# Performance work log

Hardware: AMD Instinct MI355X
Metric: run time of the kernel (lower is better)

## Reference

```python
import jax, jax.numpy as jnp
import numpy as np

N = 50000          # nodes
E = 1600000        # edges (avg degree 32)
B = 64             # graphs in batch
IN_CH = 128
HEADS = 8
HD = 8             # head_dim = ceil(64/8)
GH = HEADS * HD    # 64 = gat_hidden_dim
HIDDEN = 64
NC = 10
NEG_SLOPE = 0.2
BN_EPS = 1e-5
SIGMA = 0.5


def setup_inputs() -> dict:
    key = jax.random.key(0)
    ks = jax.random.split(key, 24)
    s = 0.1
    inp = {
        "x": jax.random.normal(ks[0], (N, IN_CH), jnp.float32),
        "raw_x": jax.random.uniform(ks[1], (N, 3), jnp.float32),
        "edge_index": jax.random.randint(ks[2], (2, E), 0, N, jnp.int32),
        "batch": jnp.sort(jax.random.randint(ks[3], (N,), 0, B, jnp.int32)),
        # conv1 (heads=8, out=8, edge_dim=1)
        "W1": jax.random.normal(ks[4], (IN_CH, GH), jnp.float32) * s,
        "att_src1": jax.random.normal(ks[5], (HEADS, HD), jnp.float32) * s,
        "att_dst1": jax.random.normal(ks[6], (HEADS, HD), jnp.float32) * s,
        "We1": jax.random.normal(ks[7], (1, GH), jnp.float32) * s,
        "att_e1": jax.random.normal(ks[8], (HEADS, HD), jnp.float32) * s,
        "b1": jax.random.normal(ks[9], (GH,), jnp.float32) * s,
        "gamma1": jnp.ones((GH,), jnp.float32),
        "beta1": jnp.zeros((GH,), jnp.float32),
        "rm1": jax.random.normal(ks[10], (GH,), jnp.float32) * s,
        "rv1": jax.random.uniform(ks[11], (GH,), jnp.float32) + 0.5,
        # conv2 (heads=1, out=64, edge_dim=1)
        "W2": jax.random.normal(ks[12], (GH, HIDDEN), jnp.float32) * s,
        "att_src2": jax.random.normal(ks[13], (1, HIDDEN), jnp.float32) * s,
        "att_dst2": jax.random.normal(ks[14], (1, HIDDEN), jnp.float32) * s,
        "We2": jax.random.normal(ks[15], (1, HIDDEN), jnp.float32) * s,
        "att_e2": jax.random.normal(ks[16], (1, HIDDEN), jnp.float32) * s,
        "b2": jax.random.normal(ks[17], (HIDDEN,), jnp.float32) * s,
        "gamma2": jnp.ones((HIDDEN,), jnp.float32),
        "beta2": jnp.zeros((HIDDEN,), jnp.float32),
        "rm2": jax.random.normal(ks[18], (HIDDEN,), jnp.float32) * s,
        "rv2": jax.random.uniform(ks[19], (HIDDEN,), jnp.float32) + 0.5,
        # classifier
        "Wc": jax.random.normal(ks[20], (HIDDEN, NC), jnp.float32) * s,
        "bc": jax.random.normal(ks[21], (NC,), jnp.float32) * s,
    }
    return inp


def _gat_conv(x, src, dst, edge_attr, W, a_src, a_dst, W_e, a_e, bias, heads, out_ch, n):
    """PyG GATConv (concat=True, add_self_loops=True, fill_value='mean', eval mode)."""
    e0 = edge_attr.shape[0]
    # self-loop edge_attr = mean of incoming edge_attr per node (0 if isolated)
    cnt = jax.ops.segment_sum(jnp.ones((e0,), x.dtype), dst, num_segments=n)
    loop_attr = jax.ops.segment_sum(edge_attr, dst, num_segments=n) / jnp.maximum(cnt, 1.0)[:, None]
    loops = jnp.arange(n, dtype=src.dtype)
    src2 = jnp.concatenate([src, loops])
    dst2 = jnp.concatenate([dst, loops])
    ea = jnp.concatenate([edge_attr, loop_attr], axis=0)          # [E2, 1]
    h = (x @ W).reshape(n, heads, out_ch)                          # [N, H, D]
    al_s = (h * a_src).sum(-1)                                     # [N, H]
    al_d = (h * a_dst).sum(-1)                                     # [N, H]
    al_e = ((ea @ W_e).reshape(-1, heads, out_ch) * a_e).sum(-1)   # [E2, H]
    logits = al_s[src2] + al_d[dst2] + al_e                        # [E2, H]
    logits = jnp.where(logits >= 0, logits, NEG_SLOPE * logits)    # leaky_relu
    # segment softmax over destination nodes (every node has a self loop)
    m = jax.ops.segment_max(logits, dst2, num_segments=n)
    ex = jnp.exp(logits - m[dst2])
    alpha = ex / jax.ops.segment_sum(ex, dst2, num_segments=n)[dst2]
    out = jax.ops.segment_sum(h[src2] * alpha[:, :, None], dst2, num_segments=n)
    return out.reshape(n, heads * out_ch) + bias


def _bn_eval(x, gamma, beta, rm, rv):
    return (x - rm) * (gamma / jnp.sqrt(rv + BN_EPS)) + beta


def reference(x, raw_x, edge_index, batch,
              W1, att_src1, att_dst1, We1, att_e1, b1, gamma1, beta1, rm1, rv1,
              W2, att_src2, att_dst2, We2, att_e2, b2, gamma2, beta2, rm2, rv2,
              Wc, bc):
    src, dst = edge_index[0], edge_index[1]
    # gaussian edge weights from raw features
    diff = raw_x[src] - raw_x[dst]
    dist2 = (diff * diff).sum(axis=1)
    edge_w = jnp.exp(-dist2 / (2.0 * SIGMA * SIGMA))[:, None]      # [E, 1]
    # eval mode: dropout is identity
    h = _gat_conv(x, src, dst, edge_w, W1, att_src1, att_dst1, We1, att_e1, b1, HEADS, HD, N)
    h = jax.nn.elu(_bn_eval(h, gamma1, beta1, rm1, rv1))
    h = _gat_conv(h, src, dst, edge_w, W2, att_src2, att_dst2, We2, att_e2, b2, 1, HIDDEN, N)
    h = jax.nn.elu(_bn_eval(h, gamma2, beta2, rm2, rv2))
    # global mean pool over graphs
    cnt = jax.ops.segment_sum(jnp.ones((N,), h.dtype), batch, num_segments=B)
    g = jax.ops.segment_sum(h, batch, num_segments=B) / jnp.maximum(cnt, 1.0)[:, None]
    return g @ Wc + bc
```

## Files before the change

kernel.cpp:

```cpp
#include <hip/hip_runtime.h>
#include <math.h>

#define N_NODES 50000
#define N_EDGES 1600000
#define NBATCH  64
#define INCH    128
#define HEADS   8
#define HD      8
#define GH      64
#define HIDDEN  64
#define NC      10
#define NEG_SLOPE 0.2f
#define BN_EPS  1e-5f

#define SCAN_TPB 1024
#define NTILES   ((N_NODES + SCAN_TPB - 1) / SCAN_TPB)

typedef unsigned short ushort_t;
typedef unsigned int uint_t;

__device__ __forceinline__ ushort_t f2bf(float f) {
  uint_t u = __float_as_uint(f);
  uint_t r = (u + 0x7fffu + ((u >> 16) & 1u)) >> 16;
  return (ushort_t)r;
}
__device__ __forceinline__ float2 upk(uint_t u) {
  return make_float2(__uint_as_float(u << 16), __uint_as_float(u & 0xffff0000u));
}

__global__ __launch_bounds__(256) void edge_kernel(
    const int* __restrict__ ei, const float* __restrict__ raw,
    float* __restrict__ ea, float* __restrict__ easum, int* __restrict__ cnt) {
  int e = blockIdx.x * blockDim.x + threadIdx.x;
  if (e >= N_EDGES) return;
  int s = ei[e], d = ei[N_EDGES + e];
  float dx = raw[s*3+0] - raw[d*3+0];
  float dy = raw[s*3+1] - raw[d*3+1];
  float dz = raw[s*3+2] - raw[d*3+2];
  float w = __expf(-2.0f * (dx*dx + dy*dy + dz*dz));
  ea[e] = w;
  atomicAdd(&easum[d], w);
  atomicAdd(&cnt[d], 1);
}

__global__ __launch_bounds__(SCAN_TPB) void scan_part(
    const int* __restrict__ cnt, const float* __restrict__ easum,
    int* __restrict__ rowptr, float* __restrict__ loopat, int* __restrict__ bsum) {
  __shared__ int s[SCAN_TPB];
  int t = threadIdx.x;
  int i = blockIdx.x * SCAN_TPB + t;
  int v = (i < N_NODES) ? cnt[i] : 0;
  s[t] = v; __syncthreads();
  for (int off = 1; off < SCAN_TPB; off <<= 1) {
    int u = (t >= off) ? s[t - off] : 0;
    __syncthreads();
    s[t] += u;
    __syncthreads();
  }
  if (i < N_NODES) {
    rowptr[i] = s[t] - v;
    loopat[i] = easum[i] / fmaxf((float)v, 1.0f);
  }
  if (t == SCAN_TPB - 1) bsum[blockIdx.x] = s[t];
}

__global__ __launch_bounds__(64) void scan_top(int* __restrict__ bsum, int* __restrict__ rowptr) {
  int t = threadIdx.x;
  int v = (t < NTILES) ? bsum[t] : 0;
  int orig = v;
  for (int off = 1; off < 64; off <<= 1) {
    int u = __shfl_up(v, off);
    if (t >= off) v += u;
  }
  if (t < NTILES) bsum[t] = v - orig;
  if (t == 0) rowptr[N_NODES] = N_EDGES;
}

__global__ __launch_bounds__(SCAN_TPB) void scan_add(int* __restrict__ rowptr, const int* __restrict__ bsum) {
  int i = blockIdx.x * SCAN_TPB + threadIdx.x;
  if (i < N_NODES) rowptr[i] += bsum[blockIdx.x];
}

__global__ __launch_bounds__(256) void scatter_kernel(
    const int* __restrict__ ei, const float* __restrict__ ea,
    const int* __restrict__ rowptr, int* __restrict__ cnt2,
    int* __restrict__ csr_src, float* __restrict__ csr_ea) {
  int e = blockIdx.x * blockDim.x + threadIdx.x;
  if (e >= N_EDGES) return;
  int s = ei[e], d = ei[N_EDGES + e];
  int pos = rowptr[d] + atomicAdd(&cnt2[d], 1);
  csr_src[pos] = s;
  csr_ea[pos] = ea[e];
}

__global__ __launch_bounds__(256) void gemm1_kernel(
    const float* __restrict__ x, const float* __restrict__ W1,
    ushort_t* __restrict__ h1b) {
  __shared__ float w[INCH * GH];
  for (int i = threadIdx.x; i < INCH * GH / 4; i += blockDim.x)
    ((float4*)w)[i] = ((const float4*)W1)[i];
  __syncthreads();
  int lane = threadIdx.x & 63;
  int waveG = __builtin_amdgcn_readfirstlane((blockIdx.x * blockDim.x + threadIdx.x) >> 6);
  int nWaves = (gridDim.x * blockDim.x) >> 6;
  for (int base = waveG * 4; base < N_NODES; base += nWaves * 4) {
    float acc[4] = {0.f, 0.f, 0.f, 0.f};
    #pragma unroll 8
    for (int k = 0; k < INCH; ++k) {
      float wv = w[k * GH + lane];
      #pragma unroll
      for (int j = 0; j < 4; ++j)
        acc[j] = fmaf(x[(size_t)(base + j) * INCH + k], wv, acc[j]);
    }
    #pragma unroll
    for (int j = 0; j < 4; ++j)
      h1b[(size_t)(base + j) * GH + lane] = f2bf(acc[j]);
  }
}

__global__ __launch_bounds__(256) void conv1_kernel(
    const ushort_t* __restrict__ h1b,
    const float* __restrict__ asrc, const float* __restrict__ adst,
    const float* __restrict__ We, const float* __restrict__ ae,
    const int* __restrict__ rowptr,
    const int* __restrict__ csr_src, const float* __restrict__ csr_ea,
    const float* __restrict__ loopat, const float* __restrict__ bias,
    const float* __restrict__ gamma, const float* __restrict__ beta,
    const float* __restrict__ rm, const float* __restrict__ rv,
    float* __restrict__ h2) {
  __shared__ int   src_lds[4][64];
  __shared__ float ea_lds[4][64];
  int l = threadIdx.x & 63;
  int w = threadIdx.x >> 6;
  int n = blockIdx.x * 4 + w;
  if (n >= N_NODES) return;
  int i = l & 15;
  int q = l >> 4;
  const float4 as4 = ((const float4*)asrc)[i];
  const float4 ad4 = ((const float4*)adst)[i];
  float4 we4 = ((const float4*)We)[i];
  float4 ae4 = ((const float4*)ae)[i];
  float ce = we4.x*ae4.x + we4.y*ae4.y + we4.z*ae4.z + we4.w*ae4.w;
  ce += __shfl_xor(ce, 1);
  const uint2* tab = (const uint2*)h1b;
  uint2 uself = tab[(size_t)n * 16 + i];
  float2 s01 = upk(uself.x), s23 = upk(uself.y);
  float als_s = s01.x*as4.x + s01.y*as4.y + s23.x*as4.z + s23.y*as4.w;
  als_s += __shfl_xor(als_s, 1);
  float aldn  = s01.x*ad4.x + s01.y*ad4.y + s23.x*ad4.z + s23.y*ad4.w;
  aldn += __shfl_xor(aldn, 1);
  int jb = rowptr[n], je = rowptr[n + 1];
  float m = -1e30f, ssum = 0.f;
  float a0 = 0.f, a1 = 0.f, a2 = 0.f, a3 = 0.f;
  for (int cb = jb; cb < je; cb += 64) {
    int cnt = je - cb; if (cnt > 64) cnt = 64;
    int idx = cb + l;
    bool vld = l < cnt;
    src_lds[w][l] = vld ? csr_src[idx] : 0;
    ea_lds[w][l]  = vld ? csr_ea[idx] : 0.f;
    int nb = (cnt + 3) >> 2;
    int j0 = q;
    int s0 = (j0 < cnt) ? src_lds[w][j0] : 0;
    uint2 rcur = tab[(size_t)s0 * 16 + i];
    for (int b = 0; b < nb; ++b) {
      uint2 rnext = rcur;
      if (b + 1 < nb) {
        int jn = ((b + 1) << 2) + q;
        int sn = (jn < cnt) ? src_lds[w][jn] : 0;
        rnext = tab[(size_t)sn * 16 + i];
      }
      int j = (b << 2) + q;
      bool val = j < cnt;
      float eav = val ? ea_lds[w][j] : 0.f;
      float2 p01 = upk(rcur.x), p23 = upk(rcur.y);
      float dp = p01.x*as4.x + p01.y*as4.y + p23.x*as4.z + p23.y*as4.w;
      dp += __shfl_xor(dp, 1);
      float lg = dp + aldn + eav * ce;
      lg = (lg >= 0.f) ? lg : NEG_SLOPE * lg;
      lg = val ? lg : -1e30f;
      float bm = fmaxf(lg, __shfl_xor(lg, 16));
      bm = fmaxf(bm, __shfl_xor(bm, 32));
      float nm = fmaxf(m, bm);
      float sc = __expf(m - nm);
      float p  = __expf(lg - nm);
      float ps = p;
      ps += __shfl_xor(ps, 16);
      ps += __shfl_xor(ps, 32);
      ssum = ssum * sc + ps;
      m = nm;
      a0 = a0 * sc + p * p01.x;
      a1 = a1 * sc + p * p01.y;
      a2 = a2 * sc + p * p23.x;
      a3 = a3 * sc + p * p23.y;
      rcur = rnext;
    }
  }
  a0 += __shfl_xor(a0, 16); a0 += __shfl_xor(a0, 32);
  a1 += __shfl_xor(a1, 16); a1 += __shfl_xor(a1, 32);
  a2 += __shfl_xor(a2, 16); a2 += __shfl_xor(a2, 32);
  a3 += __shfl_xor(a3, 16); a3 += __shfl_xor(a3, 32);
  {
    float lg = als_s + aldn + loopat[n] * ce;
    lg = (lg >= 0.f) ? lg : NEG_SLOPE * lg;
    float nm = fmaxf(m, lg);
    float sc = __expf(m - nm);
    float p  = __expf(lg - nm);
    ssum = ssum * sc + p;
    a0 = a0 * sc + p * s01.x;
    a1 = a1 * sc + p * s01.y;
    a2 = a2 * sc + p * s23.x;
    a3 = a3 * sc + p * s23.y;
  }
  float inv = 1.0f / ssum;
  float4 b4 = ((const float4*)bias)[i];
  float4 g4 = ((const float4*)gamma)[i];
  float4 be4 = ((const float4*)beta)[i];
  float4 rm4 = ((const float4*)rm)[i];
  float4 rv4 = ((const float4*)rv)[i];
  float o0 = a0 * inv + b4.x, o1 = a1 * inv + b4.y;
  float o2 = a2 * inv + b4.z, o3 = a3 * inv + b4.w;
  o0 = (o0 - rm4.x) * (g4.x * rsqrtf(rv4.x + BN_EPS)) + be4.x;
  o1 = (o1 - rm4.y) * (g4.y * rsqrtf(rv4.y + BN_EPS)) + be4.y;
  o2 = (o2 - rm4.z) * (g4.z * rsqrtf(rv4.z + BN_EPS)) + be4.z;
  o3 = (o3 - rm4.w) * (g4.w * rsqrtf(rv4.w + BN_EPS)) + be4.w;
  o0 = (o0 > 0.f) ? o0 : expm1f(o0);
  o1 = (o1 > 0.f) ? o1 : expm1f(o1);
  o2 = (o2 > 0.f) ? o2 : expm1f(o2);
  o3 = (o3 > 0.f) ? o3 : expm1f(o3);
  if (q == 0)
    ((float4*)(h2 + (size_t)n * GH))[i] = make_float4(o0, o1, o2, o3);
}

__global__ __launch_bounds__(256) void gemm2_kernel(
    const float* __restrict__ x, const float* __restrict__ W2,
    ushort_t* __restrict__ h2mb) {
  __shared__ float w[HIDDEN * HIDDEN];
  for (int i = threadIdx.x; i < HIDDEN * HIDDEN / 4; i += blockDim.x)
    ((float4*)w)[i] = ((const float4*)W2)[i];
  __syncthreads();
  int lane = threadIdx.x & 63;
  int waveG = __builtin_amdgcn_readfirstlane((blockIdx.x * blockDim.x + threadIdx.x) >> 6);
  int nWaves = (gridDim.x * blockDim.x) >> 6;
  for (int base = waveG * 4; base < N_NODES; base += nWaves * 4) {
    float acc[4] = {0.f, 0.f, 0.f, 0.f};
    #pragma unroll 8
    for (int k = 0; k < HIDDEN; ++k) {
      float wv = w[k * HIDDEN + lane];
      #pragma unroll
      for (int j = 0; j < 4; ++j)
        acc[j] = fmaf(x[(size_t)(base + j) * HIDDEN + k], wv, acc[j]);
    }
    #pragma unroll
    for (int j = 0; j < 4; ++j)
      h2mb[(size_t)(base + j) * HIDDEN + lane] = f2bf(acc[j]);
  }
}

__global__ __launch_bounds__(256) void conv2_kernel(
    const ushort_t* __restrict__ h2mb,
    const float* __restrict__ asrc, const float* __restrict__ adst,
    const float* __restrict__ We, const float* __restrict__ ae,
    const int* __restrict__ rowptr,
    const int* __restrict__ csr_src, const float* __restrict__ csr_ea,
    const float* __restrict__ loopat, const float* __restrict__ bias,
    const float* __restrict__ gamma, const float* __restrict__ beta,
    const float* __restrict__ rm, const float* __restrict__ rv,
    const int* __restrict__ batch,
    float* __restrict__ pool, int* __restrict__ cntg) {
  __shared__ int   src_lds[4][64];
  __shared__ float ea_lds[4][64];
  int l = threadIdx.x & 63;
  int w = threadIdx.x >> 6;
  int n = blockIdx.x * 4 + w;
  if (n >= N_NODES) return;
  int i = l & 15;
  int q = l >> 4;
  const float4 as4 = ((const float4*)asrc)[i];
  const float4 ad4 = ((const float4*)adst)[i];
  float4 we4 = ((const float4*)We)[i];
  float4 ae4 = ((const float4*)ae)[i];
  float ce = we4.x*ae4.x + we4.y*ae4.y + we4.z*ae4.z + we4.w*ae4.w;
  ce += __shfl_xor(ce, 1); ce += __shfl_xor(ce, 2);
  ce += __shfl_xor(ce, 4); ce += __shfl_xor(ce, 8);
  const uint2* tab = (const uint2*)h2mb;
  uint2 uself = tab[(size_t)n * 16 + i];
  float2 s01 = upk(uself.x), s23 = upk(uself.y);
  float als_s = s01.x*as4.x + s01.y*as4.y + s23.x*as4.z + s23.y*as4.w;
  als_s += __shfl_xor(als_s, 1); als_s += __shfl_xor(als_s, 2);
  als_s += __shfl_xor(als_s, 4); als_s += __shfl_xor(als_s, 8);
  float aldn  = s01.x*ad4.x + s01.y*ad4.y + s23.x*ad4.z + s23.y*ad4.w;
  aldn += __shfl_xor(aldn, 1); aldn += __shfl_xor(aldn, 2);
  aldn += __shfl_xor(aldn, 4); aldn += __shfl_xor(aldn, 8);
  int jb = rowptr[n], je = rowptr[n + 1];
  float m = -1e30f, ssum = 0.f;
  float a0 = 0.f, a1 = 0.f, a2 = 0.f, a3 = 0.f;
  for (int cb = jb; cb < je; cb += 64) {
    int cnt = je - cb; if (cnt > 64) cnt = 64;
    int idx = cb + l;
    bool vld = l < cnt;
    src_lds[w][l] = vld ? csr_src[idx] : 0;
    ea_lds[w][l]  = vld ? csr_ea[idx] : 0.f;
    int nb = (cnt + 3) >> 2;
    int j0 = q;
    int s0 = (j0 < cnt) ? src_lds[w][j0] : 0;
    uint2 rcur = tab[(size_t)s0 * 16 + i];
    for (int b = 0; b < nb; ++b) {
      uint2 rnext = rcur;
      if (b + 1 < nb) {
        int jn = ((b + 1) << 2) + q;
        int sn = (jn < cnt) ? src_lds[w][jn] : 0;
        rnext = tab[(size_t)sn * 16 + i];
      }
      int j = (b << 2) + q;
      bool val = j < cnt;
      float eav = val ? ea_lds[w][j] : 0.f;
      float2 p01 = upk(rcur.x), p23 = upk(rcur.y);
      float dp = p01.x*as4.x + p01.y*as4.y + p23.x*as4.z + p23.y*as4.w;
      dp += __shfl_xor(dp, 1); dp += __shfl_xor(dp, 2);
      dp += __shfl_xor(dp, 4); dp += __shfl_xor(dp, 8);
      float lg = dp + aldn + eav * ce;
      lg = (lg >= 0.f) ? lg : NEG_SLOPE * lg;
      lg = val ? lg : -1e30f;
      float bm = fmaxf(lg, __shfl_xor(lg, 16));
      bm = fmaxf(bm, __shfl_xor(bm, 32));
      float nm = fmaxf(m, bm);
      float sc = __expf(m - nm);
      float p  = __expf(lg - nm);
      float ps = p;
      ps += __shfl_xor(ps, 16);
      ps += __shfl_xor(ps, 32);
      ssum = ssum * sc + ps;
      m = nm;
      a0 = a0 * sc + p * p01.x;
      a1 = a1 * sc + p * p01.y;
      a2 = a2 * sc + p * p23.x;
      a3 = a3 * sc + p * p23.y;
      rcur = rnext;
    }
  }
  a0 += __shfl_xor(a0, 16); a0 += __shfl_xor(a0, 32);
  a1 += __shfl_xor(a1, 16); a1 += __shfl_xor(a1, 32);
  a2 += __shfl_xor(a2, 16); a2 += __shfl_xor(a2, 32);
  a3 += __shfl_xor(a3, 16); a3 += __shfl_xor(a3, 32);
  {
    float lg = als_s + aldn + loopat[n] * ce;
    lg = (lg >= 0.f) ? lg : NEG_SLOPE * lg;
    float nm = fmaxf(m, lg);
    float sc = __expf(m - nm);
    float p  = __expf(lg - nm);
    ssum = ssum * sc + p;
    a0 = a0 * sc + p * s01.x;
    a1 = a1 * sc + p * s01.y;
    a2 = a2 * sc + p * s23.x;
    a3 = a3 * sc + p * s23.y;
  }
  float inv = 1.0f / ssum;
  float4 b4 = ((const float4*)bias)[i];
  float4 g4 = ((const float4*)gamma)[i];
  float4 be4 = ((const float4*)beta)[i];
  float4 rm4 = ((const float4*)rm)[i];
  float4 rv4 = ((const float4*)rv)[i];
  float o0 = a0 * inv + b4.x, o1 = a1 * inv + b4.y;
  float o2 = a2 * inv + b4.z, o3 = a3 * inv + b4.w;
  o0 = (o0 - rm4.x) * (g4.x * rsqrtf(rv4.x + BN_EPS)) + be4.x;
  o1 = (o1 - rm4.y) * (g4.y * rsqrtf(rv4.y + BN_EPS)) + be4.y;
  o2 = (o2 - rm4.z) * (g4.z * rsqrtf(rv4.z + BN_EPS)) + be4.z;
  o3 = (o3 - rm4.w) * (g4.w * rsqrtf(rv4.w + BN_EPS)) + be4.w;
  o0 = (o0 > 0.f) ? o0 : expm1f(o0);
  o1 = (o1 > 0.f) ? o1 : expm1f(o1);
  o2 = (o2 > 0.f) ? o2 : expm1f(o2);
  o3 = (o3 > 0.f) ? o3 : expm1f(o3);
  if (q == 0) {
    int b = batch[n];
    float* pp = pool + (size_t)b * HIDDEN + 4 * i;
    atomicAdd(pp + 0, o0);
    atomicAdd(pp + 1, o1);
    atomicAdd(pp + 2, o2);
    atomicAdd(pp + 3, o3);
    if (l == 0) atomicAdd(&cntg[b], 1);
  }
}

__global__ __launch_bounds__(640) void final_kernel(
    const float* __restrict__ pool, const int* __restrict__ cntg,
    const float* __restrict__ Wc, const float* __restrict__ bc,
    float* __restrict__ out) {
  int t = threadIdx.x;
  if (t >= NBATCH * NC) return;
  int b = t / NC, c = t - b * NC;
  float inv = 1.0f / fmaxf((float)cntg[b], 1.0f);
  float s = bc[c];
  #pragma unroll
  for (int d = 0; d < HIDDEN; ++d)
    s = fmaf(pool[b * HIDDEN + d] * inv, Wc[d * NC + c], s);
  out[t] = s;
}

extern "C" void kernel_launch(void* const* d_in, const int* in_sizes, int n_in,
                              void* d_out, int out_size, void* d_ws, size_t ws_size,
                              hipStream_t stream) {
  const float* x     = (const float*)d_in[0];
  const float* raw   = (const float*)d_in[1];
  const int*   ei    = (const int*)  d_in[2];
  const int*   batch = (const int*)  d_in[3];
  const float* W1    = (const float*)d_in[4];
  const float* asrc1 = (const float*)d_in[5];
  const float* adst1 = (const float*)d_in[6];
  const float* We1   = (const float*)d_in[7];
  const float* ae1   = (const float*)d_in[8];
  const float* b1    = (const float*)d_in[9];
  const float* g1    = (const float*)d_in[10];
  const float* be1   = (const float*)d_in[11];
  const float* rm1   = (const float*)d_in[12];
  const float* rv1   = (const float*)d_in[13];
  const float* W2    = (const float*)d_in[14];
  const float* asrc2 = (const float*)d_in[15];
  const float* adst2 = (const float*)d_in[16];
  const float* We2   = (const float*)d_in[17];
  const float* ae2   = (const float*)d_in[18];
  const float* b2    = (const float*)d_in[19];
  const float* g2    = (const float*)d_in[20];
  const float* be2   = (const float*)d_in[21];
  const float* rm2   = (const float*)d_in[22];
  const float* rv2   = (const float*)d_in[23];
  const float* Wc    = (const float*)d_in[24];
  const float* bc    = (const float*)d_in[25];
  float* out = (float*)d_out;

  char* ws = (char*)d_ws;
  size_t off = 0;
  auto alloc = [&](size_t bytes) -> void* {
    void* p = ws + off;
    off += bytes;
    off = (off + 255) & ~(size_t)255;
    return p;
  };
  float*    ea      = (float*)   alloc((size_t)N_EDGES * 4);
  float*    csr_ea  = (float*)   alloc((size_t)N_EDGES * 4);
  int*      csr_src = (int*)     alloc((size_t)N_EDGES * 4);
  float*    easum   = (float*)   alloc((size_t)N_NODES * 4);
  int*      cnt     = (int*)     alloc((size_t)N_NODES * 4);
  int*      cnt2    = (int*)     alloc((size_t)N_NODES * 4);
  int*      rowptr  = (int*)     alloc((size_t)(N_NODES + 1) * 4);
  float*    loopat  = (float*)   alloc((size_t)N_NODES * 4);
  ushort_t* h1b     = (ushort_t*)alloc((size_t)N_NODES * GH * 2);
  float*    h2      = (float*)   alloc((size_t)N_NODES * GH * 4);
  ushort_t* h2mb    = (ushort_t*)alloc((size_t)N_NODES * HIDDEN * 2);
  int*      bsum    = (int*)     alloc(64 * 4);
  float*    pool    = (float*)   alloc((size_t)NBATCH * HIDDEN * 4);
  int*      cntg    = (int*)     alloc((size_t)NBATCH * 4);

  hipMemsetAsync(easum, 0, (size_t)N_NODES * 4, stream);
  hipMemsetAsync(cnt,   0, (size_t)N_NODES * 4, stream);
  hipMemsetAsync(cnt2,  0, (size_t)N_NODES * 4, stream);
  hipMemsetAsync(pool,  0, (size_t)NBATCH * HIDDEN * 4, stream);
  hipMemsetAsync(cntg,  0, (size_t)NBATCH * 4, stream);

  int egrid = (N_EDGES + 255) / 256;
  edge_kernel<<<egrid, 256, 0, stream>>>(ei, raw, ea, easum, cnt);
  scan_part<<<NTILES, SCAN_TPB, 0, stream>>>(cnt, easum, rowptr, loopat, bsum);
  scan_top<<<1, 64, 0, stream>>>(bsum, rowptr);
  scan_add<<<NTILES, SCAN_TPB, 0, stream>>>(rowptr, bsum);
  scatter_kernel<<<egrid, 256, 0, stream>>>(ei, ea, rowptr, cnt2, csr_src, csr_ea);

  gemm1_kernel<<<1024, 256, 0, stream>>>(x, W1, h1b);
  conv1_kernel<<<(N_NODES + 3) / 4, 256, 0, stream>>>(h1b, asrc1, adst1, We1, ae1,
      rowptr, csr_src, csr_ea, loopat, b1, g1, be1, rm1, rv1, h2);
  gemm2_kernel<<<1024, 256, 0, stream>>>(h2, W2, h2mb);
  conv2_kernel<<<(N_NODES + 3) / 4, 256, 0, stream>>>(h2mb, asrc2, adst2, We2, ae2,
      rowptr, csr_src, csr_ea, loopat, b2, g2, be2, rm2, rv2, batch, pool, cntg);
  final_kernel<<<1, 640, 0, stream>>>(pool, cntg, Wc, bc, out);
}
```

Measured before the change: 929.9 us.

## Precompute per-node attention scores in GEMMs and drop online softmax max tracking

```diff
diff --git a/kernel.cpp b/kernel.cpp
--- a/kernel.cpp
+++ b/kernel.cpp
@@ -95,7 +95,8 @@
 
 __global__ __launch_bounds__(256) void gemm1_kernel(
     const float* __restrict__ x, const float* __restrict__ W1,
-    ushort_t* __restrict__ h1b) {
+    const float* __restrict__ asrc, const float* __restrict__ adst,
+    ushort_t* __restrict__ h1b, float* __restrict__ als, float* __restrict__ ald) {
   __shared__ float w[INCH * GH];
   for (int i = threadIdx.x; i < INCH * GH / 4; i += blockDim.x)
     ((float4*)w)[i] = ((const float4*)W1)[i];
@@ -103,6 +104,8 @@
   int lane = threadIdx.x & 63;
   int waveG = __builtin_amdgcn_readfirstlane((blockIdx.x * blockDim.x + threadIdx.x) >> 6);
   int nWaves = (gridDim.x * blockDim.x) >> 6;
+  float a_s = asrc[lane];
+  float a_d = adst[lane];
   for (int base = waveG * 4; base < N_NODES; base += nWaves * 4) {
     float acc[4] = {0.f, 0.f, 0.f, 0.f};
     #pragma unroll 8
@@ -113,14 +116,24 @@
         acc[j] = fmaf(x[(size_t)(base + j) * INCH + k], wv, acc[j]);
     }
     #pragma unroll
-    for (int j = 0; j < 4; ++j)
-      h1b[(size_t)(base + j) * GH + lane] = f2bf(acc[j]);
+    for (int j = 0; j < 4; ++j) {
+      int n = base + j;
+      float hv = acc[j];
+      h1b[(size_t)n * GH + lane] = f2bf(hv);
+      float ps = hv * a_s, pd = hv * a_d;
+      ps += __shfl_xor(ps, 1); ps += __shfl_xor(ps, 2); ps += __shfl_xor(ps, 4);
+      pd += __shfl_xor(pd, 1); pd += __shfl_xor(pd, 2); pd += __shfl_xor(pd, 4);
+      if ((lane & 7) == 0) {
+        als[n * HEADS + (lane >> 3)] = ps;
+        ald[n * HEADS + (lane >> 3)] = pd;
+      }
+    }
   }
 }
 
 __global__ __launch_bounds__(256) void conv1_kernel(
-    const ushort_t* __restrict__ h1b,
-    const float* __restrict__ asrc, const float* __restrict__ adst,
+    const ushort_t* __restrict__ h1b, const float* __restrict__ als,
+    const float* __restrict__ ald,
     const float* __restrict__ We, const float* __restrict__ ae,
     const int* __restrict__ rowptr,
     const int* __restrict__ csr_src, const float* __restrict__ csr_ea,
@@ -136,104 +149,111 @@
   if (n >= N_NODES) return;
   int i = l & 15;
   int q = l >> 4;
-  const float4 as4 = ((const float4*)asrc)[i];
-  const float4 ad4 = ((const float4*)adst)[i];
+  int head = i >> 1;
   float4 we4 = ((const float4*)We)[i];
   float4 ae4 = ((const float4*)ae)[i];
   float ce = we4.x*ae4.x + we4.y*ae4.y + we4.z*ae4.z + we4.w*ae4.w;
   ce += __shfl_xor(ce, 1);
+  float aldn = ald[(size_t)n * HEADS + head];
+  float als_self = als[(size_t)n * HEADS + head];
   const uint2* tab = (const uint2*)h1b;
   uint2 uself = tab[(size_t)n * 16 + i];
   float2 s01 = upk(uself.x), s23 = upk(uself.y);
-  float als_s = s01.x*as4.x + s01.y*as4.y + s23.x*as4.z + s23.y*as4.w;
-  als_s += __shfl_xor(als_s, 1);
-  float aldn  = s01.x*ad4.x + s01.y*ad4.y + s23.x*ad4.z + s23.y*ad4.w;
-  aldn += __shfl_xor(aldn, 1);
   int jb = rowptr[n], je = rowptr[n + 1];
-  float m = -1e30f, ssum = 0.f;
+  float ssum = 0.f;
   float a0 = 0.f, a1 = 0.f, a2 = 0.f, a3 = 0.f;
+
+#define C1_LOADS(J, R, A, E)                                           \
+  {                                                                    \
+    int jj = (J);                                                      \
+    bool vv = jj < cnt;                                                \
+    int ss = vv ? src_lds[w][jj] : 0;                                  \
+    R = tab[(size_t)ss * 16 + i];                                      \
+    A = vv ? als[(size_t)ss * HEADS + head] : -1e30f;                  \
+    E = vv ? ea_lds[w][jj] : 0.f;                                      \
+  }
+#define C1_LOADG(GI, R0,R1,R2,R3, A0,A1,A2,A3, E0,E1,E2,E3)            \
+  {                                                                    \
+    int jbase = (GI) * 16 + q;                                         \
+    C1_LOADS(jbase,      R0, A0, E0)                                   \
+    C1_LOADS(jbase + 4,  R1, A1, E1)                                   \
+    C1_LOADS(jbase + 8,  R2, A2, E2)                                   \
+    C1_LOADS(jbase + 12, R3, A3, E3)                                   \
+  }
+#define C1_PROC(R, A, E)                                               \
+  {                                                                    \
+    float2 t01 = upk(R.x), t23 = upk(R.y);                             \
+    float lg = A + aldn + E * ce;                                      \
+    lg = (lg >= 0.f) ? lg : NEG_SLOPE * lg;                            \
+    float p = __expf(fminf(lg, 60.f));                                 \
+    ssum += p;                                                         \
+    a0 = fmaf(p, t01.x, a0); a1 = fmaf(p, t01.y, a1);                  \
+    a2 = fmaf(p, t23.x, a2); a3 = fmaf(p, t23.y, a3);                  \
+  }
+
   for (int cb = jb; cb < je; cb += 64) {
     int cnt = je - cb; if (cnt > 64) cnt = 64;
-    int idx = cb + l;
-    bool vld = l < cnt;
-    src_lds[w][l] = vld ? csr_src[idx] : 0;
-    ea_lds[w][l]  = vld ? csr_ea[idx] : 0.f;
-    int nb = (cnt + 3) >> 2;
-    int j0 = q;
-    int s0 = (j0 < cnt) ? src_lds[w][j0] : 0;
-    uint2 rcur = tab[(size_t)s0 * 16 + i];
-    for (int b = 0; b < nb; ++b) {
-      uint2 rnext = rcur;
-      if (b + 1 < nb) {
-        int jn = ((b + 1) << 2) + q;
-        int sn = (jn < cnt) ? src_lds[w][jn] : 0;
-        rnext = tab[(size_t)sn * 16 + i];
+    src_lds[w][l] = (l < cnt) ? csr_src[cb + l] : 0;
+    ea_lds[w][l]  = (l < cnt) ? csr_ea[cb + l] : 0.f;
+    int ng = (cnt + 15) >> 4;
+    uint2 rA0, rA1, rA2, rA3, rB0, rB1, rB2, rB3;
+    float aA0, aA1, aA2, aA3, aB0, aB1, aB2, aB3;
+    float eA0, eA1, eA2, eA3, eB0, eB1, eB2, eB3;
+    C1_LOADG(0, rA0,rA1,rA2,rA3, aA0,aA1,aA2,aA3, eA0,eA1,eA2,eA3)
+    for (int gi = 0; gi < ng; gi += 2) {
+      bool hasB = (gi + 1) < ng;
+      if (hasB) C1_LOADG(gi + 1, rB0,rB1,rB2,rB3, aB0,aB1,aB2,aB3, eB0,eB1,eB2,eB3)
+      C1_PROC(rA0, aA0, eA0) C1_PROC(rA1, aA1, eA1)
+      C1_PROC(rA2, aA2, eA2) C1_PROC(rA3, aA3, eA3)
+      if (hasB) {
+        if (gi + 2 < ng) C1_LOADG(gi + 2, rA0,rA1,rA2,rA3, aA0,aA1,aA2,aA3, eA0,eA1,eA2,eA3)
+        C1_PROC(rB0, aB0, eB0) C1_PROC(rB1, aB1, eB1)
+        C1_PROC(rB2, aB2, eB2) C1_PROC(rB3, aB3, eB3)
       }
-      int j = (b << 2) + q;
-      bool val = j < cnt;
-      float eav = val ? ea_lds[w][j] : 0.f;
-      float2 p01 = upk(rcur.x), p23 = upk(rcur.y);
-      float dp = p01.x*as4.x + p01.y*as4.y + p23.x*as4.z + p23.y*as4.w;
-      dp += __shfl_xor(dp, 1);
-      float lg = dp + aldn + eav * ce;
-      lg = (lg >= 0.f) ? lg : NEG_SLOPE * lg;
-      lg = val ? lg : -1e30f;
-      float bm = fmaxf(lg, __shfl_xor(lg, 16));
-      bm = fmaxf(bm, __shfl_xor(bm, 32));
-      float nm = fmaxf(m, bm);
-      float sc = __expf(m - nm);
-      float p  = __expf(lg - nm);
-      float ps = p;
-      ps += __shfl_xor(ps, 16);
-      ps += __shfl_xor(ps, 32);
-      ssum = ssum * sc + ps;
-      m = nm;
-      a0 = a0 * sc + p * p01.x;
-      a1 = a1 * sc + p * p01.y;
-      a2 = a2 * sc + p * p23.x;
-      a3 = a3 * sc + p * p23.y;
-      rcur = rnext;
     }
   }
+#undef C1_LOADS
+#undef C1_LOADG
+#undef C1_PROC
+
+  ssum += __shfl_xor(ssum, 16); ssum += __shfl_xor(ssum, 32);
   a0 += __shfl_xor(a0, 16); a0 += __shfl_xor(a0, 32);
   a1 += __shfl_xor(a1, 16); a1 += __shfl_xor(a1, 32);
   a2 += __shfl_xor(a2, 16); a2 += __shfl_xor(a2, 32);
   a3 += __shfl_xor(a3, 16); a3 += __shfl_xor(a3, 32);
   {
-    float lg = als_s + aldn + loopat[n] * ce;
+    float lg = als_self + aldn + loopat[n] * ce;
     lg = (lg >= 0.f) ? lg : NEG_SLOPE * lg;
-    float nm = fmaxf(m, lg);
-    float sc = __expf(m - nm);
-    float p  = __expf(lg - nm);
-    ssum = ssum * sc + p;
-    a0 = a0 * sc + p * s01.x;
-    a1 = a1 * sc + p * s01.y;
-    a2 = a2 * sc + p * s23.x;
-    a3 = a3 * sc + p * s23.y;
-  }
-  float inv = 1.0f / ssum;
-  float4 b4 = ((const float4*)bias)[i];
-  float4 g4 = ((const float4*)gamma)[i];
-  float4 be4 = ((const float4*)beta)[i];
-  float4 rm4 = ((const float4*)rm)[i];
-  float4 rv4 = ((const float4*)rv)[i];
-  float o0 = a0 * inv + b4.x, o1 = a1 * inv + b4.y;
-  float o2 = a2 * inv + b4.z, o3 = a3 * inv + b4.w;
-  o0 = (o0 - rm4.x) * (g4.x * rsqrtf(rv4.x + BN_EPS)) + be4.x;
-  o1 = (o1 - rm4.y) * (g4.y * rsqrtf(rv4.y + BN_EPS)) + be4.y;
-  o2 = (o2 - rm4.z) * (g4.z * rsqrtf(rv4.z + BN_EPS)) + be4.z;
-  o3 = (o3 - rm4.w) * (g4.w * rsqrtf(rv4.w + BN_EPS)) + be4.w;
-  o0 = (o0 > 0.f) ? o0 : expm1f(o0);
-  o1 = (o1 > 0.f) ? o1 : expm1f(o1);
-  o2 = (o2 > 0.f) ? o2 : expm1f(o2);
-  o3 = (o3 > 0.f) ? o3 : expm1f(o3);
-  if (q == 0)
+    float p = __expf(fminf(lg, 60.f));
+    ssum += p;
+    a0 = fmaf(p, s01.x, a0); a1 = fmaf(p, s01.y, a1);
+    a2 = fmaf(p, s23.x, a2); a3 = fmaf(p, s23.y, a3);
+  }
+  if (q == 0) {
+    float inv = 1.0f / ssum;
+    float4 b4 = ((const float4*)bias)[i];
+    float4 g4 = ((const float4*)gamma)[i];
+    float4 be4 = ((const float4*)beta)[i];
+    float4 rm4 = ((const float4*)rm)[i];
+    float4 rv4 = ((const float4*)rv)[i];
+    float o0 = a0 * inv + b4.x, o1 = a1 * inv + b4.y;
+    float o2 = a2 * inv + b4.z, o3 = a3 * inv + b4.w;
+    o0 = (o0 - rm4.x) * (g4.x * rsqrtf(rv4.x + BN_EPS)) + be4.x;
+    o1 = (o1 - rm4.y) * (g4.y * rsqrtf(rv4.y + BN_EPS)) + be4.y;
+    o2 = (o2 - rm4.z) * (g4.z * rsqrtf(rv4.z + BN_EPS)) + be4.z;
+    o3 = (o3 - rm4.w) * (g4.w * rsqrtf(rv4.w + BN_EPS)) + be4.w;
+    o0 = (o0 > 0.f) ? o0 : expm1f(o0);
+    o1 = (o1 > 0.f) ? o1 : expm1f(o1);
+    o2 = (o2 > 0.f) ? o2 : expm1f(o2);
+    o3 = (o3 > 0.f) ? o3 : expm1f(o3);
     ((float4*)(h2 + (size_t)n * GH))[i] = make_float4(o0, o1, o2, o3);
+  }
 }
 
 __global__ __launch_bounds__(256) void gemm2_kernel(
     const float* __restrict__ x, const float* __restrict__ W2,
-    ushort_t* __restrict__ h2mb) {
+    const float* __restrict__ asrc, const float* __restrict__ adst,
+    ushort_t* __restrict__ h2mb, float* __restrict__ als, float* __restrict__ ald) {
   __shared__ float w[HIDDEN * HIDDEN];
   for (int i = threadIdx.x; i < HIDDEN * HIDDEN / 4; i += blockDim.x)
     ((float4*)w)[i] = ((const float4*)W2)[i];
@@ -241,6 +261,8 @@
   int lane = threadIdx.x & 63;
   int waveG = __builtin_amdgcn_readfirstlane((blockIdx.x * blockDim.x + threadIdx.x) >> 6);
   int nWaves = (gridDim.x * blockDim.x) >> 6;
+  float a_s = asrc[lane];
+  float a_d = adst[lane];
   for (int base = waveG * 4; base < N_NODES; base += nWaves * 4) {
     float acc[4] = {0.f, 0.f, 0.f, 0.f};
     #pragma unroll 8
@@ -251,14 +273,24 @@
         acc[j] = fmaf(x[(size_t)(base + j) * HIDDEN + k], wv, acc[j]);
     }
     #pragma unroll
-    for (int j = 0; j < 4; ++j)
-      h2mb[(size_t)(base + j) * HIDDEN + lane] = f2bf(acc[j]);
+    for (int j = 0; j < 4; ++j) {
+      int n = base + j;
+      float hv = acc[j];
+      h2mb[(size_t)n * HIDDEN + lane] = f2bf(hv);
+      float ps = hv * a_s, pd = hv * a_d;
+      #pragma unroll
+      for (int off = 1; off < 64; off <<= 1) {
+        ps += __shfl_xor(ps, off);
+        pd += __shfl_xor(pd, off);
+      }
+      if (lane == 0) { als[n] = ps; ald[n] = pd; }
+    }
   }
 }
 
 __global__ __launch_bounds__(256) void conv2_kernel(
-    const ushort_t* __restrict__ h2mb,
-    const float* __restrict__ asrc, const float* __restrict__ adst,
+    const ushort_t* __restrict__ h2mb, const float* __restrict__ als,
+    const float* __restrict__ ald,
     const float* __restrict__ We, const float* __restrict__ ae,
     const int* __restrict__ rowptr,
     const int* __restrict__ csr_src, const float* __restrict__ csr_ea,
@@ -275,102 +307,103 @@
   if (n >= N_NODES) return;
   int i = l & 15;
   int q = l >> 4;
-  const float4 as4 = ((const float4*)asrc)[i];
-  const float4 ad4 = ((const float4*)adst)[i];
   float4 we4 = ((const float4*)We)[i];
   float4 ae4 = ((const float4*)ae)[i];
   float ce = we4.x*ae4.x + we4.y*ae4.y + we4.z*ae4.z + we4.w*ae4.w;
   ce += __shfl_xor(ce, 1); ce += __shfl_xor(ce, 2);
   ce += __shfl_xor(ce, 4); ce += __shfl_xor(ce, 8);
+  float aldn = ald[n];
+  float als_self = als[n];
   const uint2* tab = (const uint2*)h2mb;
   uint2 uself = tab[(size_t)n * 16 + i];
   float2 s01 = upk(uself.x), s23 = upk(uself.y);
-  float als_s = s01.x*as4.x + s01.y*as4.y + s23.x*as4.z + s23.y*as4.w;
-  als_s += __shfl_xor(als_s, 1); als_s += __shfl_xor(als_s, 2);
-  als_s += __shfl_xor(als_s, 4); als_s += __shfl_xor(als_s, 8);
-  float aldn  = s01.x*ad4.x + s01.y*ad4.y + s23.x*ad4.z + s23.y*ad4.w;
-  aldn += __shfl_xor(aldn, 1); aldn += __shfl_xor(aldn, 2);
-  aldn += __shfl_xor(aldn, 4); aldn += __shfl_xor(aldn, 8);
   int jb = rowptr[n], je = rowptr[n + 1];
-  float m = -1e30f, ssum = 0.f;
+  float ssum = 0.f;
   float a0 = 0.f, a1 = 0.f, a2 = 0.f, a3 = 0.f;
+
+#define C2_LOADS(J, R, A, E)                                           \
+  {                                                                    \
+    int jj = (J);                                                      \
+    bool vv = jj < cnt;                                                \
+    int ss = vv ? src_lds[w][jj] : 0;                                  \
+    R = tab[(size_t)ss * 16 + i];                                      \
+    A = vv ? als[ss] : -1e30f;                                         \
+    E = vv ? ea_lds[w][jj] : 0.f;                                      \
+  }
+#define C2_LOADG(GI, R0,R1,R2,R3, A0,A1,A2,A3, E0,E1,E2,E3)            \
+  {                                                                    \
+    int jbase = (GI) * 16 + q;                                         \
+    C2_LOADS(jbase,      R0, A0, E0)                                   \
+    C2_LOADS(jbase + 4,  R1, A1, E1)                                   \
+    C2_LOADS(jbase + 8,  R2, A2, E2)                                   \
+    C2_LOADS(jbase + 12, R3, A3, E3)                                   \
+  }
+#define C2_PROC(R, A, E)                                               \
+  {                                                                    \
+    float2 t01 = upk(R.x), t23 = upk(R.y);                             \
+    float lg = A + aldn + E * ce;                                      \
+    lg = (lg >= 0.f) ? lg : NEG_SLOPE * lg;                            \
+    float p = __expf(fminf(lg, 60.f));                                 \
+    ssum += p;                                                         \
+    a0 = fmaf(p, t01.x, a0); a1 = fmaf(p, t01.y, a1);                  \
+    a2 = fmaf(p, t23.x, a2); a3 = fmaf(p, t23.y, a3);                  \
+  }
+
   for (int cb = jb; cb < je; cb += 64) {
     int cnt = je - cb; if (cnt > 64) cnt = 64;
-    int idx = cb + l;
-    bool vld = l < cnt;
-    src_lds[w][l] = vld ? csr_src[idx] : 0;
-    ea_lds[w][l]  = vld ? csr_ea[idx] : 0.f;
-    int nb = (cnt + 3) >> 2;
-    int j0 = q;
-    int s0 = (j0 < cnt) ? src_lds[w][j0] : 0;
-    uint2 rcur = tab[(size_t)s0 * 16 + i];
-    for (int b = 0; b < nb; ++b) {
-      uint2 rnext = rcur;
-      if (b + 1 < nb) {
-        int jn = ((b + 1) << 2) + q;
-        int sn = (jn < cnt) ? src_lds[w][jn] : 0;
-        rnext = tab[(size_t)sn * 16 + i];
+    src_lds[w][l] = (l < cnt) ? csr_src[cb + l] : 0;
+    ea_lds[w][l]  = (l < cnt) ? csr_ea[cb + l] : 0.f;
+    int ng = (cnt + 15) >> 4;
+    uint2 rA0, rA1, rA2, rA3, rB0, rB1, rB2, rB3;
+    float aA0, aA1, aA2, aA3, aB0, aB1, aB2, aB3;
+    float eA0, eA1, eA2, eA3, eB0, eB1, eB2, eB3;
+    C2_LOADG(0, rA0,rA1,rA2,rA3, aA0,aA1,aA2,aA3, eA0,eA1,eA2,eA3)
+    for (int gi = 0; gi < ng; gi += 2) {
+      bool hasB = (gi + 1) < ng;
+      if (hasB) C2_LOADG(gi + 1, rB0,rB1,rB2,rB3, aB0,aB1,aB2,aB3, eB0,eB1,eB2,eB3)
+      C2_PROC(rA0, aA0, eA0) C2_PROC(rA1, aA1, eA1)
+      C2_PROC(rA2, aA2, eA2) C2_PROC(rA3, aA3, eA3)
+      if (hasB) {
+        if (gi + 2 < ng) C2_LOADG(gi + 2, rA0,rA1,rA2,rA3, aA0,aA1,aA2,aA3, eA0,eA1,eA2,eA3)
+        C2_PROC(rB0, aB0, eB0) C2_PROC(rB1, aB1, eB1)
+        C2_PROC(rB2, aB2, eB2) C2_PROC(rB3, aB3, eB3)
       }
-      int j = (b << 2) + q;
-      bool val = j < cnt;
-      float eav = val ? ea_lds[w][j] : 0.f;
-      float2 p01 = upk(rcur.x), p23 = upk(rcur.y);
-      float dp = p01.x*as4.x + p01.y*as4.y + p23.x*as4.z + p23.y*as4.w;
-      dp += __shfl_xor(dp, 1); dp += __shfl_xor(dp, 2);
-      dp += __shfl_xor(dp, 4); dp += __shfl_xor(dp, 8);
-      float lg = dp + aldn + eav * ce;
-      lg = (lg >= 0.f) ? lg : NEG_SLOPE * lg;
-      lg = val ? lg : -1e30f;
-      float bm = fmaxf(lg, __shfl_xor(lg, 16));
-      bm = fmaxf(bm, __shfl_xor(bm, 32));
-      float nm = fmaxf(m, bm);
-      float sc = __expf(m - nm);
-      float p  = __expf(lg - nm);
-      float ps = p;
-      ps += __shfl_xor(ps, 16);
-      ps += __shfl_xor(ps, 32);
-      ssum = ssum * sc + ps;
-      m = nm;
-      a0 = a0 * sc + p * p01.x;
-      a1 = a1 * sc + p * p01.y;
-      a2 = a2 * sc + p * p23.x;
-      a3 = a3 * sc + p * p23.y;
-      rcur = rnext;
     }
   }
+#undef C2_LOADS
+#undef C2_LOADG
+#undef C2_PROC
+
+  ssum += __shfl_xor(ssum, 16); ssum += __shfl_xor(ssum, 32);
   a0 += __shfl_xor(a0, 16); a0 += __shfl_xor(a0, 32);
   a1 += __shfl_xor(a1, 16); a1 += __shfl_xor(a1, 32);
   a2 += __shfl_xor(a2, 16); a2 += __shfl_xor(a2, 32);
   a3 += __shfl_xor(a3, 16); a3 += __shfl_xor(a3, 32);
   {
-    float lg = als_s + aldn + loopat[n] * ce;
+    float lg = als_self + aldn + loopat[n] * ce;
     lg = (lg >= 0.f) ? lg : NEG_SLOPE * lg;
-    float nm = fmaxf(m, lg);
-    float sc = __expf(m - nm);
-    float p  = __expf(lg - nm);
-    ssum = ssum * sc + p;
-    a0 = a0 * sc + p * s01.x;
-    a1 = a1 * sc + p * s01.y;
-    a2 = a2 * sc + p * s23.x;
-    a3 = a3 * sc + p * s23.y;
-  }
-  float inv = 1.0f / ssum;
-  float4 b4 = ((const float4*)bias)[i];
-  float4 g4 = ((const float4*)gamma)[i];
-  float4 be4 = ((const float4*)beta)[i];
-  float4 rm4 = ((const float4*)rm)[i];
-  float4 rv4 = ((const float4*)rv)[i];
-  float o0 = a0 * inv + b4.x, o1 = a1 * inv + b4.y;
-  float o2 = a2 * inv + b4.z, o3 = a3 * inv + b4.w;
-  o0 = (o0 - rm4.x) * (g4.x * rsqrtf(rv4.x + BN_EPS)) + be4.x;
-  o1 = (o1 - rm4.y) * (g4.y * rsqrtf(rv4.y + BN_EPS)) + be4.y;
-  o2 = (o2 - rm4.z) * (g4.z * rsqrtf(rv4.z + BN_EPS)) + be4.z;
-  o3 = (o3 - rm4.w) * (g4.w * rsqrtf(rv4.w + BN_EPS)) + be4.w;
-  o0 = (o0 > 0.f) ? o0 : expm1f(o0);
-  o1 = (o1 > 0.f) ? o1 : expm1f(o1);
-  o2 = (o2 > 0.f) ? o2 : expm1f(o2);
-  o3 = (o3 > 0.f) ? o3 : expm1f(o3);
+    float p = __expf(fminf(lg, 60.f));
+    ssum += p;
+    a0 = fmaf(p, s01.x, a0); a1 = fmaf(p, s01.y, a1);
+    a2 = fmaf(p, s23.x, a2); a3 = fmaf(p, s23.y, a3);
+  }
   if (q == 0) {
+    float inv = 1.0f / ssum;
+    float4 b4 = ((const float4*)bias)[i];
+    float4 g4 = ((const float4*)gamma)[i];
+    float4 be4 = ((const float4*)beta)[i];
+    float4 rm4 = ((const float4*)rm)[i];
+    float4 rv4 = ((const float4*)rv)[i];
+    float o0 = a0 * inv + b4.x, o1 = a1 * inv + b4.y;
+    float o2 = a2 * inv + b4.z, o3 = a3 * inv + b4.w;
+    o0 = (o0 - rm4.x) * (g4.x * rsqrtf(rv4.x + BN_EPS)) + be4.x;
+    o1 = (o1 - rm4.y) * (g4.y * rsqrtf(rv4.y + BN_EPS)) + be4.y;
+    o2 = (o2 - rm4.z) * (g4.z * rsqrtf(rv4.z + BN_EPS)) + be4.z;
+    o3 = (o3 - rm4.w) * (g4.w * rsqrtf(rv4.w + BN_EPS)) + be4.w;
+    o0 = (o0 > 0.f) ? o0 : expm1f(o0);
+    o1 = (o1 > 0.f) ? o1 : expm1f(o1);
+    o2 = (o2 > 0.f) ? o2 : expm1f(o2);
+    o3 = (o3 > 0.f) ? o3 : expm1f(o3);
     int b = batch[n];
     float* pp = pool + (size_t)b * HIDDEN + 4 * i;
     atomicAdd(pp + 0, o0);
@@ -444,8 +477,12 @@
   int*      rowptr  = (int*)     alloc((size_t)(N_NODES + 1) * 4);
   float*    loopat  = (float*)   alloc((size_t)N_NODES * 4);
   ushort_t* h1b     = (ushort_t*)alloc((size_t)N_NODES * GH * 2);
+  float*    als1    = (float*)   alloc((size_t)N_NODES * HEADS * 4);
+  float*    ald1    = (float*)   alloc((size_t)N_NODES * HEADS * 4);
   float*    h2      = (float*)   alloc((size_t)N_NODES * GH * 4);
   ushort_t* h2mb    = (ushort_t*)alloc((size_t)N_NODES * HIDDEN * 2);
+  float*    als2    = (float*)   alloc((size_t)N_NODES * 4);
+  float*    ald2    = (float*)   alloc((size_t)N_NODES * 4);
   int*      bsum    = (int*)     alloc(64 * 4);
   float*    pool    = (float*)   alloc((size_t)NBATCH * HIDDEN * 4);
   int*      cntg    = (int*)     alloc((size_t)NBATCH * 4);
@@ -463,11 +500,11 @@
   scan_add<<<NTILES, SCAN_TPB, 0, stream>>>(rowptr, bsum);
   scatter_kernel<<<egrid, 256, 0, stream>>>(ei, ea, rowptr, cnt2, csr_src, csr_ea);
 
-  gemm1_kernel<<<1024, 256, 0, stream>>>(x, W1, h1b);
-  conv1_kernel<<<(N_NODES + 3) / 4, 256, 0, stream>>>(h1b, asrc1, adst1, We1, ae1,
+  gemm1_kernel<<<1024, 256, 0, stream>>>(x, W1, asrc1, adst1, h1b, als1, ald1);
+  conv1_kernel<<<(N_NODES + 3) / 4, 256, 0, stream>>>(h1b, als1, ald1, We1, ae1,
       rowptr, csr_src, csr_ea, loopat, b1, g1, be1, rm1, rv1, h2);
-  gemm2_kernel<<<1024, 256, 0, stream>>>(h2, W2, h2mb);
-  conv2_kernel<<<(N_NODES + 3) / 4, 256, 0, stream>>>(h2mb, asrc2, adst2, We2, ae2,
+  gemm2_kernel<<<1024, 256, 0, stream>>>(h2, W2, asrc2, adst2, h2mb, als2, ald2);
+  conv2_kernel<<<(N_NODES + 3) / 4, 256, 0, stream>>>(h2mb, als2, ald2, We2, ae2,
       rowptr, csr_src, csr_ea, loopat, b2, g2, be2, rm2, rv2, batch, pool, cntg);
   final_kernel<<<1, 640, 0, stream>>>(pool, cntg, Wc, bc, out);
 }
```

Measured after the change: 1.005 ms. 8.1% more time.
